# Optimization experiments

Measured on AMD Instinct MI355X. Metric: run time of the kernel, lower is better.

Reference implementation:

```python
import jax, jax.numpy as jnp
import numpy as np

N = 100000          # nodes
E = 1600000         # directed edges
F_IN = 512          # num_features
H = 8               # heads
FH = 8              # per-head out channels
C = H * FH          # 64 hidden channels
HID = (2 * C) // 2  # 64, PyG JK lstm hidden size
NUM_CLASSES = 40
NEG_SLOPE = 0.2     # GATConv leaky relu slope


def setup_inputs() -> dict:
    key = jax.random.key(0)
    ks = jax.random.split(key, 24)
    s = 0.1
    inp = {
        "x": jax.random.normal(ks[0], (N, F_IN), jnp.float32),
        "edge_index": jax.random.randint(ks[1], (2, E), 0, N, jnp.int64)
        if jax.config.jax_enable_x64 else jax.random.randint(ks[1], (2, E), 0, N, jnp.int32),
        # GATConv 1
        "W1": jax.random.normal(ks[2], (F_IN, H * FH), jnp.float32) * s,
        "a1_src": jax.random.normal(ks[3], (H, FH), jnp.float32) * s,
        "a1_dst": jax.random.normal(ks[4], (H, FH), jnp.float32) * s,
        "b1": jnp.zeros((H * FH,), jnp.float32),
        # GATConv 2
        "W2": jax.random.normal(ks[5], (C, H * FH), jnp.float32) * s,
        "a2_src": jax.random.normal(ks[6], (H, FH), jnp.float32) * s,
        "a2_dst": jax.random.normal(ks[7], (H, FH), jnp.float32) * s,
        "b2": jnp.zeros((H * FH,), jnp.float32),
        # JK bidirectional LSTM (torch gate order i,f,g,o)
        "Wih_f": jax.random.normal(ks[8], (4 * HID, C), jnp.float32) * s,
        "Whh_f": jax.random.normal(ks[9], (4 * HID, HID), jnp.float32) * s,
        "bih_f": jnp.zeros((4 * HID,), jnp.float32),
        "bhh_f": jnp.zeros((4 * HID,), jnp.float32),
        "Wih_b": jax.random.normal(ks[10], (4 * HID, C), jnp.float32) * s,
        "Whh_b": jax.random.normal(ks[11], (4 * HID, HID), jnp.float32) * s,
        "bih_b": jnp.zeros((4 * HID,), jnp.float32),
        "bhh_b": jnp.zeros((4 * HID,), jnp.float32),
        # JK attention head
        "w_att": jax.random.normal(ks[12], (2 * HID,), jnp.float32) * s,
        "b_att": jnp.zeros((), jnp.float32),
        # output layer (bias=False)
        "W_out": jax.random.normal(ks[13], (NUM_CLASSES, C), jnp.float32) * s,
    }
    return inp


def gat_layer(x, src, dst, W, a_src, a_dst, b):
    n = x.shape[0]
    h = (x @ W).reshape(n, H, FH)                       # [N,H,FH]
    al_s = jnp.einsum('nhf,hf->nh', h, a_src)           # [N,H]
    al_d = jnp.einsum('nhf,hf->nh', h, a_dst)
    e = jax.nn.leaky_relu(al_s[src] + al_d[dst], NEG_SLOPE)  # [E',H]
    m = jax.ops.segment_max(e, dst, num_segments=n)     # segment softmax over dst
    ex = jnp.exp(e - m[dst])
    ssum = jax.ops.segment_sum(ex, dst, num_segments=n)
    alpha = ex / ssum[dst]                              # [E',H]
    out = jax.ops.segment_sum(h[src] * alpha[:, :, None], dst, num_segments=n)
    return out.reshape(n, H * FH) + b


def lstm_dir(xs, Wih, Whh, bih, bhh):
    # xs: [L, N, C] -> hs: [L, N, HID]
    n = xs.shape[1]

    def step(carry, xt):
        hprev, cprev = carry
        g = xt @ Wih.T + bih + hprev @ Whh.T + bhh
        i, f, gg, o = jnp.split(g, 4, axis=-1)
        c = jax.nn.sigmoid(f) * cprev + jax.nn.sigmoid(i) * jnp.tanh(gg)
        hh = jax.nn.sigmoid(o) * jnp.tanh(c)
        return (hh, c), hh

    init = (jnp.zeros((n, HID), xs.dtype), jnp.zeros((n, HID), xs.dtype))
    _, hs = jax.lax.scan(step, init, xs)
    return hs


def reference(x, edge_index, W1, a1_src, a1_dst, b1, W2, a2_src, a2_dst, b2,
              Wih_f, Whh_f, bih_f, bhh_f, Wih_b, Whh_b, bih_b, bhh_b,
              w_att, b_att, W_out):
    n = x.shape[0]
    loop = jnp.arange(n, dtype=edge_index.dtype)        # PyG add_self_loops
    src = jnp.concatenate([edge_index[0], loop])
    dst = jnp.concatenate([edge_index[1], loop])

    # eval mode: dropouts are identity
    x1 = jax.nn.elu(gat_layer(x, src, dst, W1, a1_src, a1_dst, b1))   # [N,64]
    x2 = gat_layer(x1, src, dst, W2, a2_src, a2_dst, b2)              # [N,64]

    xs = jnp.stack([x1, x2], axis=0)                    # [L=2, N, 64]
    h_f = lstm_dir(xs, Wih_f, Whh_f, bih_f, bhh_f)
    h_b = lstm_dir(xs[::-1], Wih_b, Whh_b, bih_b, bhh_b)[::-1]
    hcat = jnp.concatenate([h_f, h_b], axis=-1)         # [2, N, 128]

    att = jnp.einsum('lnk,k->ln', hcat, w_att) + b_att  # [2, N]
    alpha = jax.nn.softmax(att, axis=0)
    final = jnp.sum(xs * alpha[:, :, None], axis=0)     # [N, 64]

    return jax.nn.log_softmax(final @ W_out.T, axis=-1)
```

## Files before the change

### kernel.cpp

```cpp
#include <hip/hip_runtime.h>
#include <math.h>

#define F_IN 512
#define NCLS 40
#define BSH 7
#define BNODES (1 << BSH)
#define CH 16384

typedef __attribute__((ext_vector_type(8))) short bf16x8;
typedef __attribute__((ext_vector_type(4))) float f32x4;

__device__ __forceinline__ f32x4 mfma_bf16(bf16x8 a, bf16x8 b, f32x4 c){
  return __builtin_amdgcn_mfma_f32_16x16x32_bf16(a, b, c, 0, 0, 0);
}
__device__ __forceinline__ float fsigm(float x){ return 1.f/(1.f+__expf(-x)); }
__device__ __forceinline__ float ftanh(float x){ return 1.f - 2.f/(__expf(2.f*x)+1.f); }
__device__ __forceinline__ unsigned short f2bf(float f){
  unsigned u = __float_as_uint(f);
  return (unsigned short)((u + 0x7fffu + ((u>>16)&1u)) >> 16);
}
__device__ __forceinline__ float bf2f(unsigned short h){
  return __uint_as_float(((unsigned)h) << 16);
}
__device__ __forceinline__ unsigned cvtpk(float lo, float hi){
  unsigned r;
  asm("v_cvt_pk_bf16_f32 %0, %1, %2" : "=v"(r) : "v"(lo), "v"(hi));
  return r;
}

__global__ __launch_bounds__(256) void k_pcount(const int* __restrict__ ei, int e, int n,
                                                int nb, int* __restrict__ bhist){
  __shared__ int h[1024];
  int b = blockIdx.x, t = threadIdx.x;
  for (int i = t; i < nb; i += 256) h[i] = 0;
  __syncthreads();
  int tot = e + n;
  int base = b*CH;
  int lim = min(base + CH, tot);
  for (int i = base + t; i < lim; i += 256){
    int d = (i < e) ? ei[e + i] : (i - e);
    atomicAdd(&h[d >> BSH], 1);
  }
  __syncthreads();
  for (int i = t; i < nb; i += 256) bhist[(size_t)b*nb + i] = h[i];
}

__global__ __launch_bounds__(256) void k_pscan1(int* __restrict__ bhist, int nb, int B,
                                                int* __restrict__ bcnt){
  int i = blockIdx.x*256 + threadIdx.x;
  if (i >= nb) return;
  int run = 0;
  for (int b = 0; b < B; b++){
    int v = bhist[(size_t)b*nb + i];
    bhist[(size_t)b*nb + i] = run;
    run += v;
  }
  bcnt[i] = run;
}

__global__ __launch_bounds__(256) void k_pscan2(const int* __restrict__ bcnt, int nb, int tot,
                                                int* __restrict__ bbase,
                                                int* __restrict__ rowptr, int n){
  __shared__ int sb[256];
  __shared__ int carry;
  int t = threadIdx.x;
  if (t == 0) carry = 0;
  __syncthreads();
  for (int c0 = 0; c0 < nb; c0 += 256){
    int v = (c0 + t < nb) ? bcnt[c0 + t] : 0;
    sb[t] = v; __syncthreads();
    for (int off = 1; off < 256; off <<= 1){
      int u = (t >= off) ? sb[t-off] : 0; __syncthreads();
      sb[t] += u; __syncthreads();
    }
    if (c0 + t < nb) bbase[c0 + t] = carry + sb[t] - v;
    __syncthreads();
    if (t == 0) carry += sb[255];
    __syncthreads();
  }
  if (t == 0){ bbase[nb] = carry; rowptr[n] = tot; }
}

__global__ __launch_bounds__(256) void k_pscatter(const int* __restrict__ ei, int e, int n,
                                                  int nb, const int* __restrict__ bhist,
                                                  const int* __restrict__ bbase,
                                                  unsigned* __restrict__ bedges){
  __shared__ int cur[1024];
  int b = blockIdx.x, t = threadIdx.x;
  for (int i = t; i < nb; i += 256)
    cur[i] = bbase[i] + bhist[(size_t)b*nb + i];
  __syncthreads();
  int tot = e + n;
  int base = b*CH;
  int lim = min(base + CH, tot);
  for (int i = base + t; i < lim; i += 256){
    int s, d;
    if (i < e){ s = ei[i]; d = ei[e + i]; } else { s = i - e; d = s; }
    int pos = atomicAdd(&cur[d >> BSH], 1);
    bedges[pos] = (unsigned)s | ((unsigned)(d & (BNODES-1)) << 20);
  }
}

__global__ __launch_bounds__(256) void k_bbuild(const unsigned* __restrict__ bedges,
                                                const int* __restrict__ bbase,
                                                int* __restrict__ rowptr, int* __restrict__ col, int n){
  int b = blockIdx.x;
  int t = threadIdx.x;
  __shared__ int hist[BNODES];
  __shared__ int sc[BNODES];
  __shared__ int cur[BNODES];
  int beg = bbase[b], end = bbase[b+1];
  if (t < BNODES) hist[t] = 0;
  __syncthreads();
  for (int i = beg + t; i < end; i += 256)
    atomicAdd(&hist[bedges[i] >> 20], 1);
  __syncthreads();
  int v = (t < BNODES) ? hist[t] : 0;
  if (t < BNODES) sc[t] = v;
  __syncthreads();
  for (int off = 1; off < BNODES; off <<= 1){
    int u = (t >= off && t < BNODES) ? sc[t-off] : 0;
    __syncthreads();
    if (t < BNODES) sc[t] += u;
    __syncthreads();
  }
  if (t < BNODES){
    int excl = sc[t] - v;
    int node = (b << BSH) + t;
    if (node < n) rowptr[node] = beg + excl;
    cur[t] = excl;
  }
  __syncthreads();
  for (int i = beg + t; i < end; i += 256){
    unsigned pk = bedges[i];
    int pos = atomicAdd(&cur[pk >> 20], 1);
    col[beg + pos] = (int)(pk & 0xFFFFFu);
  }
}

__global__ __launch_bounds__(256) void k_prep(
    const float* __restrict__ W1, const float* __restrict__ W2,
    const float* __restrict__ Wihf, const float* __restrict__ Whhf,
    const float* __restrict__ Wihb, const float* __restrict__ Whhb,
    unsigned short* __restrict__ W1T, unsigned short* __restrict__ W2T,
    unsigned short* __restrict__ Wfx, unsigned short* __restrict__ Wfh,
    unsigned short* __restrict__ Wbx, unsigned short* __restrict__ Wbh)
{
  int i = blockIdx.x*256 + threadIdx.x;
  if (i < 32768){
    int k = i >> 6, c = i & 63;
    W1T[c*512 + k] = f2bf(W1[i]);
  } else if (i < 36864){
    int j = i - 32768; int k = j >> 6, c = j & 63;
    W2T[c*64 + k] = f2bf(W2[j]);
  } else if (i < 102400){
    int j = i - 36864;
    int which = j >> 14, o = j & 16383;
    const float* src = which==0 ? Wihf : which==1 ? Whhf : which==2 ? Wihb : Whhb;
    unsigned short* dst = which==0 ? Wfx : which==1 ? Wfh : which==2 ? Wbx : Wbh;
    dst[o] = f2bf(src[o]);
  }
}

__global__ __launch_bounds__(256, 4) void k_gemm512(
    const float* __restrict__ Xf, const unsigned short* __restrict__ WT,
    const float* __restrict__ as_, const float* __restrict__ ad_,
    unsigned short* __restrict__ Hb, unsigned short* __restrict__ alsb,
    float* __restrict__ ald, int n)
{
  int t = threadIdx.x;
  int w = t >> 6, l = t & 63;
  int c = l & 15, kg = l >> 4;
  int n0 = blockIdx.x*64 + w*16;
  int row = min(n0 + c, n-1);
  const float* xp = Xf + (size_t)row*512 + kg*8;
  const unsigned short* wpp = WT + (size_t)c*512 + kg*8;

  f32x4 acc[4];
  #pragma unroll
  for (int j = 0; j < 4; j++) acc[j] = (f32x4){0.f,0.f,0.f,0.f};

  float4 alo[3], ahi[3];
  bf16x8 wb[3][4];
  #pragma unroll
  for (int q = 0; q < 2; q++){
    alo[q] = *reinterpret_cast<const float4*>(xp + q*32);
    ahi[q] = *reinterpret_cast<const float4*>(xp + q*32 + 4);
    #pragma unroll
    for (int j = 0; j < 4; j++)
      wb[q][j] = *reinterpret_cast<const bf16x8*>(wpp + j*8192 + q*32);
  }
  #pragma unroll
  for (int kt = 0; kt < 16; ++kt){
    int cur = kt % 3;
    int nxt = (kt + 2) % 3;
    if (kt < 14){
      alo[nxt] = *reinterpret_cast<const float4*>(xp + (kt+2)*32);
      ahi[nxt] = *reinterpret_cast<const float4*>(xp + (kt+2)*32 + 4);
      #pragma unroll
      for (int j = 0; j < 4; j++)
        wb[nxt][j] = *reinterpret_cast<const bf16x8*>(wpp + j*8192 + (kt+2)*32);
    }
    union { unsigned u[4]; bf16x8 v; } cc;
    cc.u[0] = cvtpk(alo[cur].x, alo[cur].y);
    cc.u[1] = cvtpk(alo[cur].z, alo[cur].w);
    cc.u[2] = cvtpk(ahi[cur].x, ahi[cur].y);
    cc.u[3] = cvtpk(ahi[cur].z, ahi[cur].w);
    #pragma unroll
    for (int j = 0; j < 4; j++)
      acc[j] = mfma_bf16(cc.v, wb[cur][j], acc[j]);
  }
  float asl[4], adl[4];
  #pragma unroll
  for (int j = 0; j < 4; j++){ asl[j] = as_[j*16 + c]; adl[j] = ad_[j*16 + c]; }
  #pragma unroll
  for (int j = 0; j < 4; j++){
    #pragma unroll
    for (int r = 0; r < 4; r++){
      int grow = n0 + kg*4 + r;
      float v = acc[j][r];
      if (grow < n) Hb[(size_t)grow*64 + j*16 + c] = f2bf(v);
      float sv = v*asl[j];
      float dv = v*adl[j];
      sv += __shfl_xor(sv, 1, 64); sv += __shfl_xor(sv, 2, 64); sv += __shfl_xor(sv, 4, 64);
      dv += __shfl_xor(dv, 1, 64); dv += __shfl_xor(dv, 2, 64); dv += __shfl_xor(dv, 4, 64);
      if ((c & 7) == 0 && grow < n){
        int head = j*2 + (c >> 3);
        alsb[(size_t)grow*8 + head] = f2bf(sv);
        ald [(size_t)grow*8 + head] = dv;
      }
    }
  }
}

__global__ __launch_bounds__(256) void k_gemm64(
    const unsigned short* __restrict__ Xh, const unsigned short* __restrict__ WT,
    const float* __restrict__ as_, const float* __restrict__ ad_,
    unsigned short* __restrict__ Hb, unsigned short* __restrict__ alsb,
    float* __restrict__ ald, int n)
{
  int t = threadIdx.x;
  int w = t >> 6, l = t & 63;
  int c = l & 15, kg = l >> 4;
  int n0 = blockIdx.x*64 + w*16;
  int row = min(n0 + c, n-1);
  f32x4 acc[4];
  #pragma unroll
  for (int j = 0; j < 4; j++) acc[j] = (f32x4){0.f,0.f,0.f,0.f};

  #pragma unroll
  for (int kt = 0; kt < 2; ++kt){
    int ko = kt*32 + kg*8;
    bf16x8 a = *reinterpret_cast<const bf16x8*>(Xh + (size_t)row*64 + ko);
    #pragma unroll
    for (int j = 0; j < 4; j++){
      bf16x8 b = *reinterpret_cast<const bf16x8*>(WT + (size_t)(j*16 + c)*64 + ko);
      acc[j] = mfma_bf16(a, b, acc[j]);
    }
  }
  float asl[4], adl[4];
  #pragma unroll
  for (int j = 0; j < 4; j++){ asl[j] = as_[j*16 + c]; adl[j] = ad_[j*16 + c]; }
  #pragma unroll
  for (int j = 0; j < 4; j++){
    #pragma unroll
    for (int r = 0; r < 4; r++){
      int grow = n0 + kg*4 + r;
      float v = acc[j][r];
      if (grow < n) Hb[(size_t)grow*64 + j*16 + c] = f2bf(v);
      float sv = v*asl[j];
      float dv = v*adl[j];
      sv += __shfl_xor(sv, 1, 64); sv += __shfl_xor(sv, 2, 64); sv += __shfl_xor(sv, 4, 64);
      dv += __shfl_xor(dv, 1, 64); dv += __shfl_xor(dv, 2, 64); dv += __shfl_xor(dv, 4, 64);
      if ((c & 7) == 0 && grow < n){
        int head = j*2 + (c >> 3);
        alsb[(size_t)grow*8 + head] = f2bf(sv);
        ald [(size_t)grow*8 + head] = dv;
      }
    }
  }
}

struct EdgeBuf {
  float a0, a1, a2, a3;
  uint4 h0, h1, h2, h3;
};

__device__ __forceinline__ void loadEB(EdgeBuf& b, const int* __restrict__ col,
                                       int pos, int beg, int end,
                                       const unsigned short* __restrict__ ap,
                                       const unsigned short* __restrict__ Hp){
  int s0 = (pos   < end) ? col[pos]   : col[beg];
  int s1 = (pos+1 < end) ? col[pos+1] : s0;
  int s2 = (pos+2 < end) ? col[pos+2] : s0;
  int s3 = (pos+3 < end) ? col[pos+3] : s0;
  b.a0 = bf2f(ap[s0*8]); b.a1 = bf2f(ap[s1*8]);
  b.a2 = bf2f(ap[s2*8]); b.a3 = bf2f(ap[s3*8]);
  b.h0 = *reinterpret_cast<const uint4*>(Hp + (size_t)s0*64);
  b.h1 = *reinterpret_cast<const uint4*>(Hp + (size_t)s1*64);
  b.h2 = *reinterpret_cast<const uint4*>(Hp + (size_t)s2*64);
  b.h3 = *reinterpret_cast<const uint4*>(Hp + (size_t)s3*64);
}

__device__ __forceinline__ void acc8(float (&acc)[8], float xf, uint4 g){
  acc[0] = fmaf(xf, bf2f((unsigned short)g.x), acc[0]);
  acc[1] = fmaf(xf, bf2f((unsigned short)(g.x>>16)), acc[1]);
  acc[2] = fmaf(xf, bf2f((unsigned short)g.y), acc[2]);
  acc[3] = fmaf(xf, bf2f((unsigned short)(g.y>>16)), acc[3]);
  acc[4] = fmaf(xf, bf2f((unsigned short)g.z), acc[4]);
  acc[5] = fmaf(xf, bf2f((unsigned short)(g.z>>16)), acc[5]);
  acc[6] = fmaf(xf, bf2f((unsigned short)g.w), acc[6]);
  acc[7] = fmaf(xf, bf2f((unsigned short)(g.w>>16)), acc[7]);
}

__device__ __forceinline__ void computeEB(const EdgeBuf& b, int pos, int end, float adv,
                                          float& ssum, float (&acc)[8]){
  float e0 = b.a0 + adv; e0 = (e0>0.f)?e0:0.2f*e0;
  float e1 = b.a1 + adv; e1 = (e1>0.f)?e1:0.2f*e1;
  float e2 = b.a2 + adv; e2 = (e2>0.f)?e2:0.2f*e2;
  float e3 = b.a3 + adv; e3 = (e3>0.f)?e3:0.2f*e3;
  float x0 = __expf(e0);
  float x1 = (pos+1 < end) ? __expf(e1) : 0.f;
  float x2 = (pos+2 < end) ? __expf(e2) : 0.f;
  float x3 = (pos+3 < end) ? __expf(e3) : 0.f;
  ssum += (x0 + x1) + (x2 + x3);
  acc8(acc, x0, b.h0);
  acc8(acc, x1, b.h1);
  acc8(acc, x2, b.h2);
  acc8(acc, x3, b.h3);
}

template<bool DO_ELU>
__global__ __launch_bounds__(256) void k_agg(
    const int* __restrict__ rowptr, const int* __restrict__ col,
    const unsigned short* __restrict__ Hb, const unsigned short* __restrict__ alsb,
    const float* __restrict__ ald, const float* __restrict__ bias,
    unsigned short* __restrict__ outb, int n)
{
  int grp = threadIdx.x >> 3;
  int ln  = threadIdx.x & 7;
  int node = blockIdx.x*32 + grp;
  if (node >= n) return;
  float adv = ald[node*8 + ln];
  int beg = rowptr[node], end = rowptr[node+1];
  const unsigned short* Hp = Hb + ln*8;
  const unsigned short* ap = alsb + ln;

  float acc[8];
  #pragma unroll
  for (int q = 0; q < 8; q++) acc[q] = 0.f;
  float ssum = 0.f;

  EdgeBuf A, B;
  int p = beg;
  loadEB(A, col, p,   beg, end, ap, Hp);
  loadEB(B, col, p+4, beg, end, ap, Hp);
  while (true){
    computeEB(A, p, end, adv, ssum, acc);
    if (p + 8 < end) loadEB(A, col, p+8, beg, end, ap, Hp);
    p += 4;
    if (p >= end) break;
    computeEB(B, p, end, adv, ssum, acc);
    if (p + 8 < end) loadEB(B, col, p+8, beg, end, ap, Hp);
    p += 4;
    if (p >= end) break;
  }

  float inv = 1.f/ssum;
  ushort4 pk0, pk1;
  float o[8];
  #pragma unroll
  for (int q = 0; q < 8; q++){
    o[q] = acc[q]*inv + bias[ln*8 + q];
    if (DO_ELU) o[q] = (o[q] > 0.f) ? o[q] : (__expf(o[q]) - 1.f);
  }
  pk0.x = f2bf(o[0]); pk0.y = f2bf(o[1]); pk0.z = f2bf(o[2]); pk0.w = f2bf(o[3]);
  pk1.x = f2bf(o[4]); pk1.y = f2bf(o[5]); pk1.z = f2bf(o[6]); pk1.w = f2bf(o[7]);
  *reinterpret_cast<ushort4*>(outb + (size_t)node*64 + ln*8)     = pk0;
  *reinterpret_cast<ushort4*>(outb + (size_t)node*64 + ln*8 + 4) = pk1;
}

__global__ __launch_bounds__(256) void k_lstm(
    const unsigned short* __restrict__ X1b, const unsigned short* __restrict__ X2b,
    const unsigned short* __restrict__ Wfx, const unsigned short* __restrict__ Wfh,
    const unsigned short* __restrict__ Wbx, const unsigned short* __restrict__ Wbh,
    const float* __restrict__ bihf, const float* __restrict__ bhhf,
    const float* __restrict__ bihb, const float* __restrict__ bhhb,
    const float* __restrict__ watt,
    float* __restrict__ pf0, float* __restrict__ pf1,
    float* __restrict__ pb0, float* __restrict__ pb1, int n)
{
  int dir = blockIdx.y;
  const unsigned short* X0 = dir ? X2b : X1b;
  const unsigned short* X1 = dir ? X1b : X2b;
  const unsigned short* Wx = dir ? Wbx : Wfx;
  const unsigned short* Wh = dir ? Wbh : Wfh;
  const float* bi = dir ? bihb : bihf;
  const float* bh = dir ? bhhb : bhhf;
  const float* wa = watt + dir*64;
  float* po0 = dir ? pb0 : pf0;
  float* po1 = dir ? pb1 : pf1;

  __shared__ unsigned short hls[32][72];
  __shared__ float attp[2][4][32];

  int t = threadIdx.x;
  int w = t >> 6, l = t & 63;
  int c = l & 15, kg = l >> 4;
  int n0 = blockIdx.x*32;
  int r0 = min(n0 + c, n-1);
  int r1 = min(n0 + 16 + c, n-1);

  int hid = w*16 + c;
  float bs0 = bi[hid]       + bh[hid];
  float bs1 = bi[hid + 64]  + bh[hid + 64];
  float bs2 = bi[hid + 128] + bh[hid + 128];
  float bs3 = bi[hid + 192] + bh[hid + 192];
  float wav = wa[hid];

  f32x4 acc[2][4];
  #pragma unroll
  for (int m = 0; m < 2; m++)
    #pragma unroll
    for (int g = 0; g < 4; g++) acc[m][g] = (f32x4){0.f,0.f,0.f,0.f};

  #pragma unroll
  for (int kt = 0; kt < 2; ++kt){
    int ko = kt*32 + kg*8;
    bf16x8 a0 = *reinterpret_cast<const bf16x8*>(X0 + (size_t)r0*64 + ko);
    bf16x8 a1 = *reinterpret_cast<const bf16x8*>(X0 + (size_t)r1*64 + ko);
    #pragma unroll
    for (int g = 0; g < 4; g++){
      bf16x8 b = *reinterpret_cast<const bf16x8*>(Wx + (size_t)(g*64 + hid)*64 + ko);
      acc[0][g] = mfma_bf16(a0, b, acc[0][g]);
      acc[1][g] = mfma_bf16(a1, b, acc[1][g]);
    }
  }
  float creg[2][4];
  #pragma unroll
  for (int m = 0; m < 2; m++){
    #pragma unroll
    for (int r = 0; r < 4; r++){
      int rl = m*16 + kg*4 + r;
      float gi = acc[m][0][r] + bs0;
      float gg = acc[m][2][r] + bs2;
      float go = acc[m][3][r] + bs3;
      float cc = fsigm(gi)*ftanh(gg);
      float hh = fsigm(go)*ftanh(cc);
      creg[m][r] = cc;
      hls[rl][hid] = f2bf(hh);
      float s = hh*wav;
      s += __shfl_xor(s, 1, 16);
      s += __shfl_xor(s, 2, 16);
      s += __shfl_xor(s, 4, 16);
      s += __shfl_xor(s, 8, 16);
      if (c == 0) attp[0][w][rl] = s;
    }
  }
  __syncthreads();

  #pragma unroll
  for (int m = 0; m < 2; m++)
    #pragma unroll
    for (int g = 0; g < 4; g++) acc[m][g] = (f32x4){0.f,0.f,0.f,0.f};

  #pragma unroll
  for (int kt = 0; kt < 4; ++kt){
    int ko = (kt & 1)*32 + kg*8;
    bf16x8 a0, a1;
    if (kt < 2){
      a0 = *reinterpret_cast<const bf16x8*>(X1 + (size_t)r0*64 + ko);
      a1 = *reinterpret_cast<const bf16x8*>(X1 + (size_t)r1*64 + ko);
    } else {
      a0 = *reinterpret_cast<const bf16x8*>(&hls[c][ko]);
      a1 = *reinterpret_cast<const bf16x8*>(&hls[16 + c][ko]);
    }
    const unsigned short* Wp = (kt < 2) ? Wx : Wh;
    #pragma unroll
    for (int g = 0; g < 4; g++){
      bf16x8 b = *reinterpret_cast<const bf16x8*>(Wp + (size_t)(g*64 + hid)*64 + ko);
      acc[0][g] = mfma_bf16(a0, b, acc[0][g]);
      acc[1][g] = mfma_bf16(a1, b, acc[1][g]);
    }
  }
  #pragma unroll
  for (int m = 0; m < 2; m++){
    #pragma unroll
    for (int r = 0; r < 4; r++){
      int rl = m*16 + kg*4 + r;
      float gi = acc[m][0][r] + bs0;
      float gf = acc[m][1][r] + bs1;
      float gg = acc[m][2][r] + bs2;
      float go = acc[m][3][r] + bs3;
      float cc = fsigm(gf)*creg[m][r] + fsigm(gi)*ftanh(gg);
      float hh = fsigm(go)*ftanh(cc);
      float s = hh*wav;
      s += __shfl_xor(s, 1, 16);
      s += __shfl_xor(s, 2, 16);
      s += __shfl_xor(s, 4, 16);
      s += __shfl_xor(s, 8, 16);
      if (c == 0) attp[1][w][rl] = s;
    }
  }
  __syncthreads();
  if (t < 32){
    int grow = n0 + t;
    if (grow < n) po0[grow] = attp[0][0][t] + attp[0][1][t] + attp[0][2][t] + attp[0][3][t];
  } else if (t < 64){
    int rr = t - 32;
    int grow = n0 + rr;
    if (grow < n) po1[grow] = attp[1][0][rr] + attp[1][1][rr] + attp[1][2][rr] + attp[1][3][rr];
  }
}

__global__ __launch_bounds__(256) void k_final(
    const unsigned short* __restrict__ x1b, const unsigned short* __restrict__ x2b,
    const float* __restrict__ pf0, const float* __restrict__ pf1,
    const float* __restrict__ pb0, const float* __restrict__ pb1,
    const float* __restrict__ Wout, float* __restrict__ out, int n)
{
  __shared__ __align__(16) float ws[NCLS][68];
  __shared__ __align__(16) float fs[32][68];
  int t = threadIdx.x;
  for (int i = t; i < NCLS*64; i += 256)
    ws[i>>6][i&63] = Wout[i];

  int n0 = blockIdx.x*32;
  int nd = t >> 3, q8 = t & 7;
  int g = n0 + nd;
  int eb = q8*8;
  if (g < n){
    float att0 = pf0[g] + pb1[g];
    float att1 = pf1[g] + pb0[g];
    float a0 = 1.f/(1.f + __expf(att1 - att0));
    float a1 = 1.f - a0;
    uint4 p1 = *reinterpret_cast<const uint4*>(x1b + (size_t)g*64 + eb);
    uint4 p2 = *reinterpret_cast<const uint4*>(x2b + (size_t)g*64 + eb);
    const unsigned* u1 = (const unsigned*)&p1;
    const unsigned* u2 = (const unsigned*)&p2;
    #pragma unroll
    for (int q = 0; q < 4; q++){
      float v1l = bf2f((unsigned short)u1[q]), v1h = bf2f((unsigned short)(u1[q]>>16));
      float v2l = bf2f((unsigned short)u2[q]), v2h = bf2f((unsigned short)(u2[q]>>16));
      fs[nd][eb + q*2 + 0] = a0*v1l + a1*v2l;
      fs[nd][eb + q*2 + 1] = a0*v1h + a1*v2h;
    }
  } else {
    #pragma unroll
    for (int q = 0; q < 8; q++) fs[nd][eb+q] = 0.f;
  }
  __syncthreads();

  float lg[5] = {0.f,0.f,0.f,0.f,0.f};
  #pragma unroll
  for (int k4 = 0; k4 < 16; k4++){
    float4 f = *reinterpret_cast<const float4*>(&fs[nd][k4*4]);
    #pragma unroll
    for (int q = 0; q < 5; q++){
      int cc = q8 + 8*q;
      float4 wv = *reinterpret_cast<const float4*>(&ws[cc][k4*4]);
      lg[q] = fmaf(f.x, wv.x, lg[q]);
      lg[q] = fmaf(f.y, wv.y, lg[q]);
      lg[q] = fmaf(f.z, wv.z, lg[q]);
      lg[q] = fmaf(f.w, wv.w, lg[q]);
    }
  }
  float mx = lg[0];
  #pragma unroll
  for (int q = 1; q < 5; q++) mx = fmaxf(mx, lg[q]);
  #pragma unroll
  for (int mk = 1; mk < 8; mk <<= 1) mx = fmaxf(mx, __shfl_xor(mx, mk, 64));
  float se = 0.f;
  #pragma unroll
  for (int q = 0; q < 5; q++) se += __expf(lg[q] - mx);
  #pragma unroll
  for (int mk = 1; mk < 8; mk <<= 1) se += __shfl_xor(se, mk, 64);
  float lse = __logf(se);
  if (g < n){
    #pragma unroll
    for (int q = 0; q < 5; q++)
      out[(size_t)g*NCLS + q8 + 8*q] = lg[q] - mx - lse;
  }
}

extern "C" void kernel_launch(void* const* d_in, const int* in_sizes, int n_in,
                              void* d_out, int out_size, void* d_ws, size_t ws_size,
                              hipStream_t stream)
{
  const float* x    = (const float*)d_in[0];
  const int*   ei   = (const int*)d_in[1];
  const float* W1   = (const float*)d_in[2];
  const float* a1s  = (const float*)d_in[3];
  const float* a1d  = (const float*)d_in[4];
  const float* b1   = (const float*)d_in[5];
  const float* W2   = (const float*)d_in[6];
  const float* a2s  = (const float*)d_in[7];
  const float* a2d  = (const float*)d_in[8];
  const float* b2   = (const float*)d_in[9];
  const float* Wih_f= (const float*)d_in[10];
  const float* Whh_f= (const float*)d_in[11];
  const float* bih_f= (const float*)d_in[12];
  const float* bhh_f= (const float*)d_in[13];
  const float* Wih_b= (const float*)d_in[14];
  const float* Whh_b= (const float*)d_in[15];
  const float* bih_b= (const float*)d_in[16];
  const float* bhh_b= (const float*)d_in[17];
  const float* watt = (const float*)d_in[18];
  const float* Wout = (const float*)d_in[20];
  float* out = (float*)d_out;

  int n = in_sizes[0] / F_IN;
  int e = in_sizes[1] / 2;
  int nb = (n + BNODES - 1) >> BSH;
  int B  = (e + n + CH - 1) / CH;

  char* p = (char*)d_ws;
  auto alloc = [&](size_t b)->char*{ char* r = p; p += (b + 255) & ~(size_t)255; return r; };
  int* rowptr = (int*)alloc((size_t)(n+1)*4);
  int* colidx = (int*)alloc((size_t)(e+n)*4);
  unsigned* bedges = (unsigned*)alloc((size_t)(e+n)*4);
  int* bhist  = (int*)alloc((size_t)B*nb*4);
  int* bcnt   = (int*)alloc((size_t)(nb+1)*4);
  int* bbase  = (int*)alloc((size_t)(nb+1)*4);
  unsigned short* hbuf = (unsigned short*)alloc((size_t)n*64*2);
  unsigned short* alsb = (unsigned short*)alloc((size_t)n*8*2);
  float* ald  = (float*)alloc((size_t)n*8*4);
  unsigned short* x1b = (unsigned short*)alloc((size_t)n*64*2);
  unsigned short* x2b = (unsigned short*)alloc((size_t)n*64*2);
  float* pf0 = (float*)alloc((size_t)n*4);
  float* pf1 = (float*)alloc((size_t)n*4);
  float* pb0 = (float*)alloc((size_t)n*4);
  float* pb1 = (float*)alloc((size_t)n*4);
  unsigned short* W1T = (unsigned short*)alloc((size_t)64*512*2);
  unsigned short* W2T = (unsigned short*)alloc((size_t)64*64*2);
  unsigned short* Wfx = (unsigned short*)alloc((size_t)256*64*2);
  unsigned short* Wfh = (unsigned short*)alloc((size_t)256*64*2);
  unsigned short* Wbx = (unsigned short*)alloc((size_t)256*64*2);
  unsigned short* Wbh = (unsigned short*)alloc((size_t)256*64*2);

  k_pcount<<<B, 256, 0, stream>>>(ei, e, n, nb, bhist);
  k_pscan1<<<(nb+255)/256, 256, 0, stream>>>(bhist, nb, B, bcnt);
  k_pscan2<<<1, 256, 0, stream>>>(bcnt, nb, e+n, bbase, rowptr, n);
  k_pscatter<<<B, 256, 0, stream>>>(ei, e, n, nb, bhist, bbase, bedges);
  k_bbuild<<<nb, 256, 0, stream>>>(bedges, bbase, rowptr, colidx, n);

  k_prep<<<400, 256, 0, stream>>>(W1, W2, Wih_f, Whh_f, Wih_b, Whh_b,
                                  W1T, W2T, Wfx, Wfh, Wbx, Wbh);

  int gblk = (n + 63)/64;
  k_gemm512<<<gblk, 256, 0, stream>>>(x, W1T, a1s, a1d, hbuf, alsb, ald, n);
  k_agg<true ><<<(n+31)/32, 256, 0, stream>>>(rowptr, colidx, hbuf, alsb, ald, b1, x1b, n);
  k_gemm64<<<gblk, 256, 0, stream>>>(x1b, W2T, a2s, a2d, hbuf, alsb, ald, n);
  k_agg<false><<<(n+31)/32, 256, 0, stream>>>(rowptr, colidx, hbuf, alsb, ald, b2, x2b, n);

  dim3 lgrid((n + 31)/32, 2);
  k_lstm<<<lgrid, 256, 0, stream>>>(x1b, x2b, Wfx, Wfh, Wbx, Wbh,
                                    bih_f, bhh_f, bih_b, bhh_b,
                                    watt, pf0, pf1, pb0, pb1, n);

  k_final<<<(n+3)/4, 256, 0, stream>>>(x1b, x2b, pf0, pf1, pb0, pb1, Wout, out, n);
}
```

Baseline: 505.4 us.

## Stage X tiles through double-buffered shared memory in first GAT GEMM

The 512-wide input GEMM now loads each 64-row block of X cooperatively into a double-buffered LDS tile, using coalesced 64-byte row segments per thread with register prefetch two chunks ahead. Previously each lane read scattered 32-byte pieces of its own row directly from global memory. The change targets global-load coalescing on the dominant 200MB read of X. In exchange it adds LDS traffic, a barrier per k-chunk, and a lower occupancy hint (launch bounds 2 instead of 4).

```diff
diff --git a/kernel.cpp b/kernel.cpp
--- a/kernel.cpp
+++ b/kernel.cpp
@@ -162,54 +162,69 @@
   }
 }
 
-__global__ __launch_bounds__(256, 4) void k_gemm512(
+__global__ __launch_bounds__(256, 2) void k_gemm512(
     const float* __restrict__ Xf, const unsigned short* __restrict__ WT,
     const float* __restrict__ as_, const float* __restrict__ ad_,
     unsigned short* __restrict__ Hb, unsigned short* __restrict__ alsb,
     float* __restrict__ ald, int n)
 {
+  __shared__ float xs[2][64][68];
   int t = threadIdx.x;
   int w = t >> 6, l = t & 63;
   int c = l & 15, kg = l >> 4;
-  int n0 = blockIdx.x*64 + w*16;
-  int row = min(n0 + c, n-1);
-  const float* xp = Xf + (size_t)row*512 + kg*8;
+  int n0 = blockIdx.x*64;
+
+  int sr = t >> 2;
+  int sc = (t & 3) << 4;
+  const float* srcrow = Xf + (size_t)min(n0 + sr, n-1)*512 + sc;
   const unsigned short* wpp = WT + (size_t)c*512 + kg*8;
 
   f32x4 acc[4];
   #pragma unroll
   for (int j = 0; j < 4; j++) acc[j] = (f32x4){0.f,0.f,0.f,0.f};
 
-  float4 alo[3], ahi[3];
-  bf16x8 wb[3][4];
-  #pragma unroll
-  for (int q = 0; q < 2; q++){
-    alo[q] = *reinterpret_cast<const float4*>(xp + q*32);
-    ahi[q] = *reinterpret_cast<const float4*>(xp + q*32 + 4);
-    #pragma unroll
-    for (int j = 0; j < 4; j++)
-      wb[q][j] = *reinterpret_cast<const bf16x8*>(wpp + j*8192 + q*32);
-  }
-  #pragma unroll
-  for (int kt = 0; kt < 16; ++kt){
-    int cur = kt % 3;
-    int nxt = (kt + 2) % 3;
-    if (kt < 14){
-      alo[nxt] = *reinterpret_cast<const float4*>(xp + (kt+2)*32);
-      ahi[nxt] = *reinterpret_cast<const float4*>(xp + (kt+2)*32 + 4);
+  float4 R[2][4];
+  #pragma unroll
+  for (int q = 0; q < 4; q++){
+    float4 v = *reinterpret_cast<const float4*>(srcrow + q*4);
+    *reinterpret_cast<float4*>(&xs[0][sr][sc + q*4]) = v;
+  }
+  #pragma unroll
+  for (int q = 0; q < 4; q++)
+    R[1][q] = *reinterpret_cast<const float4*>(srcrow + 64 + q*4);
+  __syncthreads();
+
+  #pragma unroll
+  for (int kt = 0; kt < 8; ++kt){
+    if (kt < 6){
       #pragma unroll
-      for (int j = 0; j < 4; j++)
-        wb[nxt][j] = *reinterpret_cast<const bf16x8*>(wpp + j*8192 + (kt+2)*32);
-    }
-    union { unsigned u[4]; bf16x8 v; } cc;
-    cc.u[0] = cvtpk(alo[cur].x, alo[cur].y);
-    cc.u[1] = cvtpk(alo[cur].z, alo[cur].w);
-    cc.u[2] = cvtpk(ahi[cur].x, ahi[cur].y);
-    cc.u[3] = cvtpk(ahi[cur].z, ahi[cur].w);
-    #pragma unroll
-    for (int j = 0; j < 4; j++)
-      acc[j] = mfma_bf16(cc.v, wb[cur][j], acc[j]);
-  }
+      for (int q = 0; q < 4; q++)
+        R[kt & 1][q] = *reinterpret_cast<const float4*>(srcrow + (kt+2)*64 + q*4);
+    }
+    #pragma unroll
+    for (int s = 0; s < 2; s++){
+      const float* xp = &xs[kt & 1][w*16 + c][s*32 + kg*8];
+      float4 u0 = *reinterpret_cast<const float4*>(xp);
+      float4 u1 = *reinterpret_cast<const float4*>(xp + 4);
+      union { unsigned u[4]; bf16x8 v; } cc;
+      cc.u[0] = cvtpk(u0.x, u0.y);
+      cc.u[1] = cvtpk(u0.z, u0.w);
+      cc.u[2] = cvtpk(u1.x, u1.y);
+      cc.u[3] = cvtpk(u1.z, u1.w);
+      #pragma unroll
+      for (int j = 0; j < 4; j++){
+        bf16x8 b = *reinterpret_cast<const bf16x8*>(wpp + j*8192 + kt*64 + s*32);
+        acc[j] = mfma_bf16(cc.v, b, acc[j]);
+      }
+    }
+    if (kt < 7){
+      #pragma unroll
+      for (int q = 0; q < 4; q++)
+        *reinterpret_cast<float4*>(&xs[(kt+1) & 1][sr][sc + q*4]) = R[(kt+1) & 1][q];
+    }
+    __syncthreads();
+  }
+
   float asl[4], adl[4];
   #pragma unroll
   for (int j = 0; j < 4; j++){ asl[j] = as_[j*16 + c]; adl[j] = ad_[j*16 + c]; }
@@ -217,7 +232,7 @@
   for (int j = 0; j < 4; j++){
     #pragma unroll
     for (int r = 0; r < 4; r++){
-      int grow = n0 + kg*4 + r;
+      int grow = n0 + w*16 + kg*4 + r;
       float v = acc[j][r];
       if (grow < n) Hb[(size_t)grow*64 + j*16 + c] = f2bf(v);
       float sv = v*asl[j];
```

Measured after the change: 550.0 us. 8.8% more time.

## Stage X tile in LDS as bf16 with swizzle before MFMA loop in gemm512

Applied to the files above, without the earlier changes.

The 512-wide projection GEMM now loads each block's 64x512 fp32 input tile with fully coalesced row-contiguous loads, converts it to bf16 and stores it into a 64 KB XOR-swizzled shared-memory buffer. The MFMA loop then reads A fragments from LDS instead of strided per-lane global loads with register software pipelining. The aim is better global coalescing for the large X read, which dominates this memory-bound kernel. In exchange, 64 KB of LDS per block lowers occupancy (launch bounds drop to 2) and removes the load/compute overlap inside a block.

```diff
diff --git a/kernel.cpp b/kernel.cpp
--- a/kernel.cpp
+++ b/kernel.cpp
@@ -162,54 +162,57 @@
   }
 }
 
-__global__ __launch_bounds__(256, 4) void k_gemm512(
+__global__ __launch_bounds__(256, 2) void k_gemm512(
     const float* __restrict__ Xf, const unsigned short* __restrict__ WT,
     const float* __restrict__ as_, const float* __restrict__ ad_,
     unsigned short* __restrict__ Hb, unsigned short* __restrict__ alsb,
     float* __restrict__ ald, int n)
 {
+  __shared__ unsigned short xs[64*512];
   int t = threadIdx.x;
+  int n0 = blockIdx.x*64;
+  char* xsb = reinterpret_cast<char*>(xs);
+
+  bool full = (n0 + 64 <= n);
+  #pragma unroll
+  for (int i = 0; i < 16; i++){
+    int g  = i*256 + t;
+    int row = g >> 6;
+    int ck  = g & 63;
+    const float* src = full ? (Xf + (size_t)(n0 + row)*512 + ck*8)
+                            : (Xf + (size_t)min(n0 + row, n-1)*512 + ck*8);
+    float4 u0 = reinterpret_cast<const float4*>(src)[0];
+    float4 u1 = reinterpret_cast<const float4*>(src)[1];
+    uint4 pk;
+    pk.x = cvtpk(u0.x, u0.y);
+    pk.y = cvtpk(u0.z, u0.w);
+    pk.z = cvtpk(u1.x, u1.y);
+    pk.w = cvtpk(u1.z, u1.w);
+    int byte = row*1024 + ((ck*16) ^ ((row & 7) << 4));
+    *reinterpret_cast<uint4*>(xsb + byte) = pk;
+  }
+  __syncthreads();
+
   int w = t >> 6, l = t & 63;
   int c = l & 15, kg = l >> 4;
-  int n0 = blockIdx.x*64 + w*16;
-  int row = min(n0 + c, n-1);
-  const float* xp = Xf + (size_t)row*512 + kg*8;
-  const unsigned short* wpp = WT + (size_t)c*512 + kg*8;
+  int row = w*16 + c;
+  const unsigned short* wp0 = WT + (size_t)c*512 + kg*8;
 
   f32x4 acc[4];
   #pragma unroll
   for (int j = 0; j < 4; j++) acc[j] = (f32x4){0.f,0.f,0.f,0.f};
 
-  float4 alo[3], ahi[3];
-  bf16x8 wb[3][4];
-  #pragma unroll
-  for (int q = 0; q < 2; q++){
-    alo[q] = *reinterpret_cast<const float4*>(xp + q*32);
-    ahi[q] = *reinterpret_cast<const float4*>(xp + q*32 + 4);
-    #pragma unroll
-    for (int j = 0; j < 4; j++)
-      wb[q][j] = *reinterpret_cast<const bf16x8*>(wpp + j*8192 + q*32);
-  }
   #pragma unroll
   for (int kt = 0; kt < 16; ++kt){
-    int cur = kt % 3;
-    int nxt = (kt + 2) % 3;
-    if (kt < 14){
-      alo[nxt] = *reinterpret_cast<const float4*>(xp + (kt+2)*32);
-      ahi[nxt] = *reinterpret_cast<const float4*>(xp + (kt+2)*32 + 4);
-      #pragma unroll
-      for (int j = 0; j < 4; j++)
-        wb[nxt][j] = *reinterpret_cast<const bf16x8*>(wpp + j*8192 + (kt+2)*32);
-    }
-    union { unsigned u[4]; bf16x8 v; } cc;
-    cc.u[0] = cvtpk(alo[cur].x, alo[cur].y);
-    cc.u[1] = cvtpk(alo[cur].z, alo[cur].w);
-    cc.u[2] = cvtpk(ahi[cur].x, ahi[cur].y);
-    cc.u[3] = cvtpk(ahi[cur].z, ahi[cur].w);
-    #pragma unroll
-    for (int j = 0; j < 4; j++)
-      acc[j] = mfma_bf16(cc.v, wb[cur][j], acc[j]);
-  }
+    int colb = (kt*64 + kg*16) ^ ((row & 7) << 4);
+    bf16x8 a = *reinterpret_cast<const bf16x8*>(xsb + row*1024 + colb);
+    #pragma unroll
+    for (int j = 0; j < 4; j++){
+      bf16x8 b = *reinterpret_cast<const bf16x8*>(wp0 + j*8192 + kt*32);
+      acc[j] = mfma_bf16(a, b, acc[j]);
+    }
+  }
+
   float asl[4], adl[4];
   #pragma unroll
   for (int j = 0; j < 4; j++){ asl[j] = as_[j*16 + c]; adl[j] = ad_[j*16 + c]; }
@@ -217,7 +220,7 @@
   for (int j = 0; j < 4; j++){
     #pragma unroll
     for (int r = 0; r < 4; r++){
-      int grow = n0 + kg*4 + r;
+      int grow = n0 + w*16 + kg*4 + r;
       float v = acc[j][r];
       if (grow < n) Hb[(size_t)grow*64 + j*16 + c] = f2bf(v);
       float sv = v*asl[j];
```

New measurement: 504.7 us. No clear change (-0.2%).
